# Kernel optimization log

Hardware: AMD Instinct MI355X
Metric: run time of the kernel (lower is better)

The kernel has to match this reference:

```python
import jax, jax.numpy as jnp
import numpy as np
import math

T, B, D, H, FF = 2048, 2, 1024, 16, 4096
HD = D // H
STD = 0.02


def _gelu(x):
    # SongNet gelu: tanh approximation
    return 0.5 * x * (1.0 + jnp.tanh(math.sqrt(2.0 / math.pi) * (x + 0.044715 * x ** 3)))


def _layer_norm(x, g, b, eps=1e-5):
    mu = jnp.mean(x, axis=-1, keepdims=True)
    var = jnp.mean((x - mu) ** 2, axis=-1, keepdims=True)
    return (x - mu) * jax.lax.rsqrt(var + eps) * g + b


def setup_inputs() -> dict:
    key = jax.random.key(0)
    ks = jax.random.split(key, 6)
    return {
        "x": jax.random.normal(ks[0], (T, B, D), jnp.float32),
        "attn_mask": jnp.triu(jnp.ones((T, T), bool), k=1),  # True = masked (causal)
        "in_proj_w": jax.random.normal(ks[1], (3 * D, D), jnp.float32) * STD,
        "in_proj_b": jnp.zeros((3 * D,), jnp.float32),
        "out_w": jax.random.normal(ks[2], (D, D), jnp.float32) * STD,
        "out_b": jnp.zeros((D,), jnp.float32),
        "fc1_w": jax.random.normal(ks[3], (FF, D), jnp.float32) * STD,
        "fc1_b": jnp.zeros((FF,), jnp.float32),
        "fc2_w": jax.random.normal(ks[4], (D, FF), jnp.float32) * STD,
        "fc2_b": jnp.zeros((D,), jnp.float32),
        "ln1_g": jnp.ones((D,), jnp.float32),
        "ln1_b": jnp.zeros((D,), jnp.float32),
        "ln2_g": jnp.ones((D,), jnp.float32),
        "ln2_b": jnp.zeros((D,), jnp.float32),
    }


def reference(x, attn_mask, in_proj_w, in_proj_b, out_w, out_b,
              fc1_w, fc1_b, fc2_w, fc2_b, ln1_g, ln1_b, ln2_g, ln2_b):
    t, b, d = x.shape
    scaling = HD ** -0.5
    # fused in-proj (qkv_same path): [T,B,3D]
    qkv = x @ in_proj_w.T + in_proj_b
    q, k, v = jnp.split(qkv, 3, axis=-1)
    q = q * scaling

    def to_heads(z):  # [T,B,D] -> [B*H, T, HD]
        return z.reshape(t, b * H, HD).transpose(1, 0, 2)

    q, k, v = to_heads(q), to_heads(k), to_heads(v)
    # [B*H, T, T] attention scores (full matrix, as in original bmm)
    scores = jnp.einsum('nth,nsh->nts', q, k)
    scores = jnp.where(attn_mask[None, :, :], -jnp.inf, scores)
    w = jax.nn.softmax(scores, axis=-1)
    attn = jnp.einsum('nts,nsh->nth', w, v)          # [B*H, T, HD]
    attn = attn.transpose(1, 0, 2).reshape(t, b, d)  # [T,B,D]
    attn = attn @ out_w.T + out_b

    h = _layer_norm(x + attn, ln1_g, ln1_b)
    ff = _gelu(h @ fc1_w.T + fc1_b) @ fc2_w.T + fc2_b
    out = _layer_norm(h + ff, ln2_g, ln2_b)
    return out
```

## Files before the change

kernel.cpp:

```cpp
#include <hip/hip_runtime.h>
#include <hip/hip_bf16.h>
#include <math.h>


typedef __bf16 bf16x8_t __attribute__((ext_vector_type(8)));
typedef __bf16 bf16x4_t __attribute__((ext_vector_type(4)));
typedef float  f32x4_t  __attribute__((ext_vector_type(4)));

#define T_  2048
#define B_  2
#define D_  1024
#define H_  16
#define HD_ 64
#define FF_ 4096
#define M_  (T_ * B_)

#define LOG2E 1.4426950408889634f
#define SCL   (0.125f * LOG2E)

__device__ __forceinline__ float gelu_f(float v) {
    const float y = 0.79788456080286535588f * (v + 0.044715f * v * v * v);
    const float t = __builtin_amdgcn_exp2f(-2.8853900817779268f * y);
    return v * __builtin_amdgcn_rcpf(1.0f + t);
}

__device__ __forceinline__ void gld_lds16(const void* g, void* l) {
    __builtin_amdgcn_global_load_lds((const __attribute__((address_space(1))) void*)g,
                                     (__attribute__((address_space(3))) void*)l, 16, 0, 0);
}

template<int MODE>
__global__ __launch_bounds__(256)
void gemm_bt(const __bf16* __restrict__ A, const __bf16* __restrict__ W,
             const float* __restrict__ bias, float* __restrict__ Cf0,
             float* __restrict__ Cf1, __bf16* __restrict__ Cb, int M, int N, int K)
{
    __shared__ __align__(16) __bf16 As[128 * 32];
    __shared__ __align__(16) __bf16 Bs[128 * 32];
    const int tid  = threadIdx.x;
    const int lane = tid & 63;
    const int wave = tid >> 6;
    const int quad = lane >> 4;
    const int l15  = lane & 15;
    const int m0 = blockIdx.y * 128;
    const int n0 = blockIdx.x * 128;
    const int wm = (wave >> 1) * 64;
    const int wn = (wave & 1) * 64;
    const int z  = blockIdx.z;
    const int Kloc = K / (int)gridDim.z;
    const int kbeg = z * Kloc;

    const int srow = wave * 32 + (lane >> 2);
    const int scol = (((lane & 3) ^ ((lane >> 3) & 3))) * 8;
    const __bf16* gA = A + (size_t)(m0 + srow) * K + scol;
    const __bf16* gB = W + (size_t)(n0 + srow) * K + scol;
    const size_t rowK16 = (size_t)16 * K;
    __bf16* ldsA0 = As + wave * 1024;
    __bf16* ldsA1 = As + wave * 1024 + 512;
    __bf16* ldsB0 = Bs + wave * 1024;
    __bf16* ldsB1 = Bs + wave * 1024 + 512;

    const int asw = (quad ^ ((l15 >> 1) & 3)) * 8;

    f32x4_t acc[4][4] = {};

    for (int kb = kbeg; kb < kbeg + Kloc; kb += 32) {
        gld_lds16(gA + kb,          ldsA0);
        gld_lds16(gA + kb + rowK16, ldsA1);
        gld_lds16(gB + kb,          ldsB0);
        gld_lds16(gB + kb + rowK16, ldsB1);
        __syncthreads();
        bf16x8_t af[4], bfr[4];
        #pragma unroll
        for (int i = 0; i < 4; ++i) af[i]  = *(const bf16x8_t*)&As[(wm + i * 16 + l15) * 32 + asw];
        #pragma unroll
        for (int i = 0; i < 4; ++i) bfr[i] = *(const bf16x8_t*)&Bs[(wn + i * 16 + l15) * 32 + asw];
        #pragma unroll
        for (int mi = 0; mi < 4; ++mi)
            #pragma unroll
            for (int ni = 0; ni < 4; ++ni)
                acc[mi][ni] = __builtin_amdgcn_mfma_f32_16x16x32_bf16(af[mi], bfr[ni], acc[mi][ni], 0, 0, 0);
        __syncthreads();
    }

    float* __restrict__ Cf = (z == 0) ? Cf0 : Cf1;
    #pragma unroll
    for (int mi = 0; mi < 4; ++mi) {
        const int row = m0 + wm + mi * 16 + quad * 4;
        #pragma unroll
        for (int ni = 0; ni < 4; ++ni) {
            const int col = n0 + wn + ni * 16 + l15;
            const float bv = (z == 0) ? bias[col] : 0.f;
            #pragma unroll
            for (int r = 0; r < 4; ++r) {
                float v = acc[mi][ni][r] + bv;
                if (MODE == 2) v = gelu_f(v);
                if (MODE == 0) Cf[(size_t)(row + r) * N + col] = v;
                else           Cb[(size_t)(row + r) * N + col] = (__bf16)v;
            }
        }
    }
}

__global__ __launch_bounds__(256)
void attn_kernel(const __bf16* __restrict__ qkv, __bf16* __restrict__ attnout)
{
    const int bh = blockIdx.y;
    const int b  = bh >> 4;
    const int h  = bh & 15;
    const int tid  = threadIdx.x;
    const int lane = tid & 63;
    const int wave = tid >> 6;
    const int quad = lane >> 4;
    const int l15  = lane & 15;

    __shared__ __align__(16) __bf16 Ks[64 * 64];
    __shared__ __align__(16) __bf16 Vt[64][72];
    __shared__ __align__(16) __bf16 Ps[4][16 * 64];

    const int kr = lane >> 3;
    const int kc = (lane & 7) ^ kr;
    const size_t krow = (size_t)B_ * 3 * D_;
    const __bf16* gK0 = qkv + ((size_t)(wave * 16 + kr) * B_ + b) * (3 * D_) + D_ + h * HD_ + kc * 8;
    __bf16* ldsK0 = &Ks[wave * 16 * 64];
    __bf16* ldsK1 = &Ks[wave * 16 * 64 + 8 * 64];
    const int ksw = l15 & 7;

    const int srow = tid >> 2;
    const int scol = (tid & 3) * 16;
    const int wcol = srow ^ ((tid & 3) << 4);

    const bf16x8_t ONES = {(__bf16)1.f, (__bf16)1.f, (__bf16)1.f, (__bf16)1.f,
                           (__bf16)1.f, (__bf16)1.f, (__bf16)1.f, (__bf16)1.f};

    for (int ph = 0; ph < 2; ++ph) {
        const int qt = (ph == 0) ? (31 - (int)blockIdx.x) : (int)blockIdx.x;
        const int q0 = qt * 64;
        const int tq = q0 + wave * 16 + l15;
        const __bf16* qbase = qkv + ((size_t)tq * B_ + b) * (3 * D_) + h * HD_;
        bf16x8_t aq0 = *(const bf16x8_t*)(qbase + quad * 8);
        bf16x8_t aq1 = *(const bf16x8_t*)(qbase + 32 + quad * 8);

        f32x4_t o[4] = {};
        f32x4_t lacc = {};

        for (int kt = 0; kt <= qt; ++kt) {
            const int s0 = kt * 64;
            __syncthreads();
            gld_lds16(gK0 + (size_t)s0 * krow,       ldsK0);
            gld_lds16(gK0 + (size_t)(s0 + 8) * krow, ldsK1);
            {
                const __bf16* vb_ = qkv + ((size_t)(s0 + srow) * B_ + b) * (3 * D_) + 2 * D_ + h * HD_ + scol;
                bf16x8_t v0 = *(const bf16x8_t*)vb_;
                bf16x8_t v1 = *(const bf16x8_t*)(vb_ + 8);
                #pragma unroll
                for (int j = 0; j < 8; ++j) Vt[scol + j][wcol]     = v0[j];
                #pragma unroll
                for (int j = 0; j < 8; ++j) Vt[scol + 8 + j][wcol] = v1[j];
            }
            __syncthreads();

            f32x4_t sc[4] = {};
            #pragma unroll
            for (int ni = 0; ni < 4; ++ni) {
                const int rb = (ni * 16 + l15) * 64;
                bf16x8_t kf0 = *(const bf16x8_t*)&Ks[rb + ((quad ^ ksw) & 7) * 8];
                bf16x8_t kf1 = *(const bf16x8_t*)&Ks[rb + (((quad + 4) ^ ksw) & 7) * 8];
                sc[ni] = __builtin_amdgcn_mfma_f32_16x16x32_bf16(aq0, kf0, sc[ni], 0, 0, 0);
                sc[ni] = __builtin_amdgcn_mfma_f32_16x16x32_bf16(aq1, kf1, sc[ni], 0, 0, 0);
            }

            const bool diag = (kt == qt);
            #pragma unroll
            for (int ni = 0; ni < 4; ++ni) {
                #pragma unroll
                for (int r = 0; r < 4; ++r) {
                    float pv = __builtin_amdgcn_exp2f(sc[ni][r] * SCL);
                    if (diag) {
                        const int tr_ = wave * 16 + quad * 4 + r;
                        pv = ((ni * 16 + l15) <= tr_) ? pv : 0.f;
                    }
                    const int row = quad * 4 + r;
                    const int ch = ((ni * 2 + (l15 >> 3)) + (row >> 1)) & 7;
                    Ps[wave][row * 64 + ch * 8 + (l15 & 7)] = (__bf16)pv;
                }
            }
            bf16x8_t ap0 = *(const bf16x8_t*)&Ps[wave][l15 * 64 + ((quad + (l15 >> 1)) & 7) * 8];
            bf16x8_t ap1 = *(const bf16x8_t*)&Ps[wave][l15 * 64 + ((quad + 4 + (l15 >> 1)) & 7) * 8];

            lacc = __builtin_amdgcn_mfma_f32_16x16x32_bf16(ap0, ONES, lacc, 0, 0, 0);
            lacc = __builtin_amdgcn_mfma_f32_16x16x32_bf16(ap1, ONES, lacc, 0, 0, 0);

            const int cb = (quad & 1) * 8;
            const int sb = quad >> 1;
            #pragma unroll
            for (int ni = 0; ni < 4; ++ni) {
                bf16x8_t bv0 = *(const bf16x8_t*)&Vt[ni * 16 + l15][cb + (((sb + 0) ^ ni) << 4)];
                bf16x8_t bv1 = *(const bf16x8_t*)&Vt[ni * 16 + l15][cb + (((sb + 2) ^ ni) << 4)];
                o[ni] = __builtin_amdgcn_mfma_f32_16x16x32_bf16(ap0, bv0, o[ni], 0, 0, 0);
                o[ni] = __builtin_amdgcn_mfma_f32_16x16x32_bf16(ap1, bv1, o[ni], 0, 0, 0);
            }
        }

        float linv[4];
        #pragma unroll
        for (int r = 0; r < 4; ++r) linv[r] = __builtin_amdgcn_rcpf(lacc[r]);
        #pragma unroll
        for (int ni = 0; ni < 4; ++ni) {
            #pragma unroll
            for (int r = 0; r < 4; ++r) {
                const int tr = q0 + wave * 16 + quad * 4 + r;
                attnout[((size_t)tr * B_ + b) * D_ + h * HD_ + ni * 16 + l15] =
                    (__bf16)(o[ni][r] * linv[r]);
            }
        }
    }
}

__global__ __launch_bounds__(256)
void ln3_kernel(const float* __restrict__ A, const float* __restrict__ R0,
                const float* __restrict__ R1,
                const float* __restrict__ g, const float* __restrict__ bb,
                float* __restrict__ outf, __bf16* __restrict__ outb)
{
    const int row = blockIdx.x;
    const int tid = threadIdx.x;
    const float4 va = ((const float4*)(A  + (size_t)row * D_))[tid];
    const float4 v0 = ((const float4*)(R0 + (size_t)row * D_))[tid];
    const float4 v1 = ((const float4*)(R1 + (size_t)row * D_))[tid];
    const float z0 = va.x + v0.x + v1.x, z1 = va.y + v0.y + v1.y;
    const float z2 = va.z + v0.z + v1.z, z3 = va.w + v0.w + v1.w;
    float s  = z0 + z1 + z2 + z3;
    float ss = z0 * z0 + z1 * z1 + z2 * z2 + z3 * z3;
    #pragma unroll
    for (int off = 1; off < 64; off <<= 1) {
        s  += __shfl_xor(s, off, 64);
        ss += __shfl_xor(ss, off, 64);
    }
    __shared__ float rs[4], rss[4];
    const int wv = tid >> 6, lane = tid & 63;
    if (lane == 0) { rs[wv] = s; rss[wv] = ss; }
    __syncthreads();
    s  = rs[0] + rs[1] + rs[2] + rs[3];
    ss = rss[0] + rss[1] + rss[2] + rss[3];
    const float mu   = s * (1.f / D_);
    const float var  = ss * (1.f / D_) - mu * mu;
    const float rstd = rsqrtf(var + 1e-5f);
    const float4 vg = ((const float4*)g)[tid];
    const float4 vb = ((const float4*)bb)[tid];
    const float o0 = (z0 - mu) * rstd * vg.x + vb.x;
    const float o1 = (z1 - mu) * rstd * vg.y + vb.y;
    const float o2 = (z2 - mu) * rstd * vg.z + vb.z;
    const float o3 = (z3 - mu) * rstd * vg.w + vb.w;
    ((float4*)(outf + (size_t)row * D_))[tid] = make_float4(o0, o1, o2, o3);
    if (outb) {
        bf16x4_t ob;
        ob[0] = (__bf16)o0; ob[1] = (__bf16)o1; ob[2] = (__bf16)o2; ob[3] = (__bf16)o3;
        ((bf16x4_t*)(outb + (size_t)row * D_))[tid] = ob;
    }
}

__global__ __launch_bounds__(256)
void cvt_kernel(const float* __restrict__ in, __bf16* __restrict__ out, int n4)
{
    const int i = blockIdx.x * 256 + threadIdx.x;
    if (i >= n4) return;
    const float4 v = ((const float4*)in)[i];
    bf16x4_t ob;
    ob[0] = (__bf16)v.x; ob[1] = (__bf16)v.y; ob[2] = (__bf16)v.z; ob[3] = (__bf16)v.w;
    ((bf16x4_t*)out)[i] = ob;
}

extern "C" void kernel_launch(void* const* d_in, const int* in_sizes, int n_in,
                              void* d_out, int out_size, void* d_ws, size_t ws_size,
                              hipStream_t stream)
{
    (void)in_sizes; (void)n_in; (void)out_size; (void)ws_size;
    const float* x         = (const float*)d_in[0];
    const float* in_proj_w = (const float*)d_in[2];
    const float* in_proj_b = (const float*)d_in[3];
    const float* out_w     = (const float*)d_in[4];
    const float* out_b     = (const float*)d_in[5];
    const float* fc1_w     = (const float*)d_in[6];
    const float* fc1_b     = (const float*)d_in[7];
    const float* fc2_w     = (const float*)d_in[8];
    const float* fc2_b     = (const float*)d_in[9];
    const float* ln1_g     = (const float*)d_in[10];
    const float* ln1_b     = (const float*)d_in[11];
    const float* ln2_g     = (const float*)d_in[12];
    const float* ln2_b     = (const float*)d_in[13];

    char* p = (char*)d_ws;
    __bf16* regA = (__bf16*)p; p += (size_t)M_ * D_ * 2;
    __bf16* hb   = (__bf16*)p; p += (size_t)M_ * D_ * 2;
    float*  yf2  = (float*)regA;
    __bf16* wreg = (__bf16*)p; p += (size_t)FF_ * D_ * 2;
    __bf16* qkvb = (__bf16*)p;
    __bf16* g1b  = qkvb;       p += (size_t)M_ * FF_ * 2;
    float*  yf   = (float*)p;  p += (size_t)M_ * D_ * 4;
    float*  hf   = (float*)p;  p += (size_t)M_ * D_ * 4;

    const dim3 blk(256);

    cvt_kernel<<<dim3((M_ * D_ / 4) / 256), blk, 0, stream>>>(x, regA, M_ * D_ / 4);
    cvt_kernel<<<dim3((3 * D_ * D_ / 4) / 256), blk, 0, stream>>>(in_proj_w, wreg, 3 * D_ * D_ / 4);
    gemm_bt<1><<<dim3(3 * D_ / 128, M_ / 128, 1), blk, 0, stream>>>(
        regA, wreg, in_proj_b, nullptr, nullptr, qkvb, M_, 3 * D_, D_);

    attn_kernel<<<dim3(T_ / 128, B_ * H_), blk, 0, stream>>>(qkvb, regA);

    cvt_kernel<<<dim3((D_ * D_ / 4) / 256), blk, 0, stream>>>(out_w, wreg, D_ * D_ / 4);
    gemm_bt<0><<<dim3(D_ / 128, M_ / 128, 2), blk, 0, stream>>>(
        regA, wreg, out_b, yf, hf, nullptr, M_, D_, D_);

    ln3_kernel<<<dim3(M_), blk, 0, stream>>>(x, yf, hf, ln1_g, ln1_b, hf, hb);

    cvt_kernel<<<dim3((FF_ * D_ / 4) / 256), blk, 0, stream>>>(fc1_w, wreg, FF_ * D_ / 4);
    gemm_bt<2><<<dim3(FF_ / 128, M_ / 128, 1), blk, 0, stream>>>(
        hb, wreg, fc1_b, nullptr, nullptr, g1b, M_, FF_, D_);

    cvt_kernel<<<dim3((D_ * FF_ / 4) / 256), blk, 0, stream>>>(fc2_w, wreg, D_ * FF_ / 4);
    gemm_bt<0><<<dim3(D_ / 128, M_ / 128, 2), blk, 0, stream>>>(
        g1b, wreg, fc2_b, yf, yf2, nullptr, M_, D_, FF_);

    ln3_kernel<<<dim3(M_), blk, 0, stream>>>(hf, yf, yf2, ln2_g, ln2_b, (float*)d_out, nullptr);
}
```

Baseline: 403.8 us.

## Pre-transpose V for async LDS loads and remap GEMM blocks across XCDs

Adds a separate kernel that writes V transposed per head into a scratch buffer. The attention kernel can then load V tiles with global_load_lds, replacing the per-iteration register transpose and scattered LDS stores. The GEMM block index is also remapped so consecutive block IDs, which are spread round-robin across the 8 XCDs, share M or N tiles for L2 reuse, and launch bounds now request 4 blocks per CU. The cost is an extra kernel launch plus a V write and read pass, and the V buffer reuses the yf scratch region.

After: 365.2 us. -9.6%, faster.

```diff
diff --git a/kernel.cpp b/kernel.cpp
--- a/kernel.cpp
+++ b/kernel.cpp
@@ -29,8 +29,8 @@
                                      (__attribute__((address_space(3))) void*)l, 16, 0, 0);
 }
 
-template<int MODE>
-__global__ __launch_bounds__(256)
+template<int MODE, int OWNM>
+__global__ __launch_bounds__(256, 4)
 void gemm_bt(const __bf16* __restrict__ A, const __bf16* __restrict__ W,
              const float* __restrict__ bias, float* __restrict__ Cf0,
              float* __restrict__ Cf1, __bf16* __restrict__ Cb, int M, int N, int K)
@@ -42,11 +42,25 @@
     const int wave = tid >> 6;
     const int quad = lane >> 4;
     const int l15  = lane & 15;
-    const int m0 = blockIdx.y * 128;
-    const int n0 = blockIdx.x * 128;
+
+    const int gx = gridDim.x, gy = gridDim.y;
+    int flat = ((int)blockIdx.z * gy + (int)blockIdx.y) * gx + (int)blockIdx.x;
+    int bx, by, z;
+    if (OWNM) {
+        const int P = gy >> 3;
+        const int x = flat & 7; int s = flat >> 3;
+        by = x * P + (s % P); s /= P;
+        bx = s % gx; z = s / gx;
+    } else {
+        const int P = gx >> 3;
+        const int x = flat & 7; int s = flat >> 3;
+        bx = x * P + (s % P); s /= P;
+        by = s % gy; z = s / gy;
+    }
+    const int m0 = by * 128;
+    const int n0 = bx * 128;
     const int wm = (wave >> 1) * 64;
     const int wn = (wave & 1) * 64;
-    const int z  = blockIdx.z;
     const int Kloc = K / (int)gridDim.z;
     const int kbeg = z * Kloc;
 
@@ -103,7 +117,31 @@
 }
 
 __global__ __launch_bounds__(256)
-void attn_kernel(const __bf16* __restrict__ qkv, __bf16* __restrict__ attnout)
+void vtrans_kernel(const __bf16* __restrict__ qkv, __bf16* __restrict__ vt)
+{
+    __shared__ __bf16 S[64][72];
+    const int tt = blockIdx.x, bh = blockIdx.y;
+    const int b = bh >> 4, h = bh & 15;
+    const int tid = threadIdx.x;
+    const int tl = tid >> 2, ch = (tid & 3) * 16;
+    const __bf16* src = qkv + ((size_t)(tt * 64 + tl) * B_ + b) * (3 * D_) + 2 * D_ + h * HD_ + ch;
+    *(bf16x8_t*)&S[tl][ch]     = *(const bf16x8_t*)src;
+    *(bf16x8_t*)&S[tl][ch + 8] = *(const bf16x8_t*)(src + 8);
+    __syncthreads();
+    #pragma unroll
+    for (int p = 0; p < 2; ++p) {
+        const int hd = p * 32 + (tid >> 3);
+        const int tc = (tid & 7) * 8;
+        bf16x8_t v;
+        #pragma unroll
+        for (int j = 0; j < 8; ++j) v[j] = S[tc + j][hd];
+        *(bf16x8_t*)(vt + ((size_t)bh * 64 + hd) * T_ + tt * 64 + tc) = v;
+    }
+}
+
+__global__ __launch_bounds__(256)
+void attn_kernel(const __bf16* __restrict__ qkv, const __bf16* __restrict__ vt,
+                 __bf16* __restrict__ attnout)
 {
     const int bh = blockIdx.y;
     const int b  = bh >> 4;
@@ -115,20 +153,19 @@
     const int l15  = lane & 15;
 
     __shared__ __align__(16) __bf16 Ks[64 * 64];
-    __shared__ __align__(16) __bf16 Vt[64][72];
+    __shared__ __align__(16) __bf16 Vs[64 * 64];
     __shared__ __align__(16) __bf16 Ps[4][16 * 64];
 
     const int kr = lane >> 3;
     const int kc = (lane & 7) ^ kr;
     const size_t krow = (size_t)B_ * 3 * D_;
     const __bf16* gK0 = qkv + ((size_t)(wave * 16 + kr) * B_ + b) * (3 * D_) + D_ + h * HD_ + kc * 8;
+    const __bf16* gV0 = vt + ((size_t)bh * 64 + wave * 16 + kr) * T_ + kc * 8;
     __bf16* ldsK0 = &Ks[wave * 16 * 64];
     __bf16* ldsK1 = &Ks[wave * 16 * 64 + 8 * 64];
+    __bf16* ldsV0 = &Vs[wave * 16 * 64];
+    __bf16* ldsV1 = &Vs[wave * 16 * 64 + 8 * 64];
     const int ksw = l15 & 7;
-
-    const int srow = tid >> 2;
-    const int scol = (tid & 3) * 16;
-    const int wcol = srow ^ ((tid & 3) << 4);
 
     const bf16x8_t ONES = {(__bf16)1.f, (__bf16)1.f, (__bf16)1.f, (__bf16)1.f,
                            (__bf16)1.f, (__bf16)1.f, (__bf16)1.f, (__bf16)1.f};
@@ -149,15 +186,8 @@
             __syncthreads();
             gld_lds16(gK0 + (size_t)s0 * krow,       ldsK0);
             gld_lds16(gK0 + (size_t)(s0 + 8) * krow, ldsK1);
-            {
-                const __bf16* vb_ = qkv + ((size_t)(s0 + srow) * B_ + b) * (3 * D_) + 2 * D_ + h * HD_ + scol;
-                bf16x8_t v0 = *(const bf16x8_t*)vb_;
-                bf16x8_t v1 = *(const bf16x8_t*)(vb_ + 8);
-                #pragma unroll
-                for (int j = 0; j < 8; ++j) Vt[scol + j][wcol]     = v0[j];
-                #pragma unroll
-                for (int j = 0; j < 8; ++j) Vt[scol + 8 + j][wcol] = v1[j];
-            }
+            gld_lds16(gV0 + s0,                      ldsV0);
+            gld_lds16(gV0 + (size_t)8 * T_ + s0,     ldsV1);
             __syncthreads();
 
             f32x4_t sc[4] = {};
@@ -191,12 +221,11 @@
             lacc = __builtin_amdgcn_mfma_f32_16x16x32_bf16(ap0, ONES, lacc, 0, 0, 0);
             lacc = __builtin_amdgcn_mfma_f32_16x16x32_bf16(ap1, ONES, lacc, 0, 0, 0);
 
-            const int cb = (quad & 1) * 8;
-            const int sb = quad >> 1;
             #pragma unroll
             for (int ni = 0; ni < 4; ++ni) {
-                bf16x8_t bv0 = *(const bf16x8_t*)&Vt[ni * 16 + l15][cb + (((sb + 0) ^ ni) << 4)];
-                bf16x8_t bv1 = *(const bf16x8_t*)&Vt[ni * 16 + l15][cb + (((sb + 2) ^ ni) << 4)];
+                const int rbv = (ni * 16 + l15) * 64;
+                bf16x8_t bv0 = *(const bf16x8_t*)&Vs[rbv + ((quad ^ ksw) & 7) * 8];
+                bf16x8_t bv1 = *(const bf16x8_t*)&Vs[rbv + (((quad + 4) ^ ksw) & 7) * 8];
                 o[ni] = __builtin_amdgcn_mfma_f32_16x16x32_bf16(ap0, bv0, o[ni], 0, 0, 0);
                 o[ni] = __builtin_amdgcn_mfma_f32_16x16x32_bf16(ap1, bv1, o[ni], 0, 0, 0);
             }
@@ -299,28 +328,30 @@
     __bf16* g1b  = qkvb;       p += (size_t)M_ * FF_ * 2;
     float*  yf   = (float*)p;  p += (size_t)M_ * D_ * 4;
     float*  hf   = (float*)p;  p += (size_t)M_ * D_ * 4;
+    __bf16* vt   = (__bf16*)yf;
 
     const dim3 blk(256);
 
     cvt_kernel<<<dim3((M_ * D_ / 4) / 256), blk, 0, stream>>>(x, regA, M_ * D_ / 4);
     cvt_kernel<<<dim3((3 * D_ * D_ / 4) / 256), blk, 0, stream>>>(in_proj_w, wreg, 3 * D_ * D_ / 4);
-    gemm_bt<1><<<dim3(3 * D_ / 128, M_ / 128, 1), blk, 0, stream>>>(
+    gemm_bt<1, 1><<<dim3(3 * D_ / 128, M_ / 128, 1), blk, 0, stream>>>(
         regA, wreg, in_proj_b, nullptr, nullptr, qkvb, M_, 3 * D_, D_);
 
-    attn_kernel<<<dim3(T_ / 128, B_ * H_), blk, 0, stream>>>(qkvb, regA);
+    vtrans_kernel<<<dim3(T_ / 64, B_ * H_), blk, 0, stream>>>(qkvb, vt);
+    attn_kernel<<<dim3(T_ / 128, B_ * H_), blk, 0, stream>>>(qkvb, vt, regA);
 
     cvt_kernel<<<dim3((D_ * D_ / 4) / 256), blk, 0, stream>>>(out_w, wreg, D_ * D_ / 4);
-    gemm_bt<0><<<dim3(D_ / 128, M_ / 128, 2), blk, 0, stream>>>(
+    gemm_bt<0, 1><<<dim3(D_ / 128, M_ / 128, 2), blk, 0, stream>>>(
         regA, wreg, out_b, yf, hf, nullptr, M_, D_, D_);
 
     ln3_kernel<<<dim3(M_), blk, 0, stream>>>(x, yf, hf, ln1_g, ln1_b, hf, hb);
 
     cvt_kernel<<<dim3((FF_ * D_ / 4) / 256), blk, 0, stream>>>(fc1_w, wreg, FF_ * D_ / 4);
-    gemm_bt<2><<<dim3(FF_ / 128, M_ / 128, 1), blk, 0, stream>>>(
+    gemm_bt<2, 0><<<dim3(FF_ / 128, M_ / 128, 1), blk, 0, stream>>>(
         hb, wreg, fc1_b, nullptr, nullptr, g1b, M_, FF_, D_);
 
     cvt_kernel<<<dim3((D_ * FF_ / 4) / 256), blk, 0, stream>>>(fc2_w, wreg, D_ * FF_ / 4);
-    gemm_bt<0><<<dim3(D_ / 128, M_ / 128, 2), blk, 0, stream>>>(
+    gemm_bt<0, 1><<<dim3(D_ / 128, M_ / 128, 2), blk, 0, stream>>>(
         g1b, wreg, fc2_b, yf, yf2, nullptr, M_, D_, FF_);
 
     ln3_kernel<<<dim3(M_), blk, 0, stream>>>(hf, yf, yf2, ln2_g, ln2_b, (float*)d_out, nullptr);
```
